# Kernel tuning notes

Measured on AMD Instinct MI355X. Metric: run time of the kernel, lower is better.

The kernel has to match this reference:

```python
import jax, jax.numpy as jnp
import numpy as np

HEAD_DIM = 64
NUM_HEADS = 16
ROPE_BASE = 10000.0


def _rope_cos_sin(seq_len, head_dim, dtype):
    inv_freq = 1.0 / (ROPE_BASE ** (jnp.arange(0, head_dim, 2, dtype=jnp.float32) / head_dim))
    t = jnp.arange(seq_len, dtype=jnp.float32)
    freqs = jnp.outer(t, inv_freq)                      # [S, D/2]
    emb = jnp.concatenate([freqs, freqs], axis=-1)      # [S, D]
    return jnp.cos(emb).astype(dtype), jnp.sin(emb).astype(dtype)


def _rotate_half(x):
    x1, x2 = jnp.split(x, 2, axis=-1)
    return jnp.concatenate([-x2, x1], axis=-1)


def setup_inputs() -> dict:
    key = jax.random.key(0)
    ks = jax.random.split(key, 5)
    B, S, H = 2, 2048, 1024
    x = jax.random.normal(ks[0], (B, S, H), dtype=jnp.float32)
    attention_mask = jnp.ones((B, S), dtype=jnp.float32)
    scale = 0.02
    Wq = jax.random.normal(ks[1], (H, H), dtype=jnp.float32) * scale
    Wk = jax.random.normal(ks[2], (H, H), dtype=jnp.float32) * scale
    Wv = jax.random.normal(ks[3], (H, H), dtype=jnp.float32) * scale
    Wo = jax.random.normal(ks[4], (H, H), dtype=jnp.float32) * scale
    return {"x": x, "attention_mask": attention_mask, "Wq": Wq, "Wk": Wk, "Wv": Wv, "Wo": Wo}


def reference(x, attention_mask, Wq, Wk, Wv, Wo):
    B, S, H = x.shape
    nh, hd = NUM_HEADS, HEAD_DIM
    scale = hd ** -0.5

    # nn.Linear semantics: y = x @ W^T  (W is [out, in])
    q = jnp.einsum('bsh,oh->bso', x, Wq).reshape(B, S, nh, hd).transpose(0, 2, 1, 3)
    k = jnp.einsum('bsh,oh->bso', x, Wk).reshape(B, S, nh, hd).transpose(0, 2, 1, 3)
    v = jnp.einsum('bsh,oh->bso', x, Wv).reshape(B, S, nh, hd).transpose(0, 2, 1, 3)

    cos, sin = _rope_cos_sin(S, hd, x.dtype)            # [S, hd]
    cos = cos[None, None, :, :]
    sin = sin[None, None, :, :]
    q = q * cos + _rotate_half(q) * sin
    k = k * cos + _rotate_half(k) * sin

    attn = jnp.einsum('bhqd,bhkd->bhqk', q, k) * scale  # [B, nh, S, S]
    mask = (1.0 - attention_mask.astype(x.dtype))[:, None, None, :] * jnp.finfo(x.dtype).min
    attn = attn + mask
    attn = jax.nn.softmax(attn, axis=-1)
    out = jnp.einsum('bhqk,bhkd->bhqd', attn, v)        # [B, nh, S, hd]
    out = out.transpose(0, 2, 1, 3).reshape(B, S, nh * hd)
    return jnp.einsum('bso,ho->bsh', out, Wo)
```

## Files before the change

kernel.cpp:

```cpp
#include <hip/hip_runtime.h>
#include <math.h>

#define BB 2
#define SS 2048
#define HH 1024
#define NH 16
#define HD 64
#define MM (BB*SS)

typedef __attribute__((ext_vector_type(8))) _Float16 f16x8;
typedef __attribute__((ext_vector_type(2))) __fp16 hf16x2;
typedef __attribute__((ext_vector_type(4))) float f32x4;

#define QSCALE 0.18033688011112042f

__device__ __forceinline__ unsigned short f2h(float f) {
    union { _Float16 h; unsigned short u; } c;
    c.h = (_Float16)f;
    return c.u;
}

__device__ __forceinline__ unsigned int pkh(float a, float b) {
    union { hf16x2 h; unsigned int u; } c;
    c.h = __builtin_amdgcn_cvt_pkrtz(a, b);
    return c.u;
}

__device__ __forceinline__ void gld16(const void* g, void* s) {
    __builtin_amdgcn_global_load_lds(
        (const __attribute__((address_space(1))) void*)g,
        (__attribute__((address_space(3))) void*)s, 16, 0, 0);
}

__global__ __launch_bounds__(256) void prep(
    const float* __restrict__ x, const float* __restrict__ mask,
    const float* __restrict__ Wq, const float* __restrict__ Wk,
    const float* __restrict__ Wv, const float* __restrict__ Wo,
    unsigned short* __restrict__ xf, unsigned short* __restrict__ wf,
    float* __restrict__ ctab, float* __restrict__ stab, float* __restrict__ mt,
    unsigned int* __restrict__ mflag)
{
    int gtid = blockIdx.x * 256 + threadIdx.x;
    if (gtid < SS * 32) {
        int s = gtid >> 5, i = gtid & 31;
        double invf = pow(10000.0, -(double)i / 32.0);
        double a = (double)s * invf;
        ctab[gtid] = (float)cos(a);
        stab[gtid] = (float)sin(a);
    }
    if (gtid < BB * SS) {
        float mv = mask[gtid];
        mt[gtid] = (1.0f - mv) * (-1.0e38f);
        unsigned long long bal = __ballot(mv == 1.0f);
        if ((threadIdx.x & 63) == 0)
            mflag[gtid >> 6] = (bal == ~0ull) ? 1u : 0u;
    }
    for (int it = gtid; it < 2097152; it += 524288) {
        float4 v; unsigned short* d; size_t off;
        if (it < 1048576) {
            off = (size_t)it * 4;
            v = *(const float4*)(x + off);
            d = xf;
        } else {
            off = (size_t)(it - 1048576) * 4;
            int row = (int)(off >> 10);
            const float* W = row < 1024 ? Wq : row < 2048 ? Wk : row < 3072 ? Wv : Wo;
            v = *(const float4*)(W + (((size_t)(row & 1023)) << 10) + (off & 1023));
            d = wf;
        }
        *(ushort4*)(d + off) = make_ushort4(f2h(v.x), f2h(v.y), f2h(v.z), f2h(v.w));
    }
}

template<int MODE>
__global__ __launch_bounds__(256, 3) void gemm3(
    const unsigned short* __restrict__ Axf,
    const unsigned short* __restrict__ Wf,
    const float* __restrict__ ctab, const float* __restrict__ stab,
    unsigned short* __restrict__ qo, unsigned short* __restrict__ ko,
    unsigned short* __restrict__ vo, float* __restrict__ fout)
{
    __shared__ __align__(16) short lsA[2][128*32];
    __shared__ __align__(16) short lsB[2][128*32];

    const int t = threadIdx.x;
    const int m0 = blockIdx.x * 128;
    const int brow0 = (MODE == 0 ? 0 : 3072) + blockIdx.y * 128;
    const int lane = t & 63, wv = t >> 6;
    const int wm = (wv >> 1) * 64, wn = (wv & 1) * 64;
    const int fr = lane & 15, fg = lane >> 4;

    const int srow = t >> 2, pc = t & 3;
    const int scx = (pc ^ ((srow >> 1) & 3)) * 8;
    const int lo  = srow * 32 + pc * 8;
    const size_t gA0 = (size_t)(m0 + srow) * HH + scx;
    const size_t gA1 = (size_t)(m0 + 64 + srow) * HH + scx;
    const size_t gB0 = (size_t)(brow0 + srow) * HH + scx;
    const size_t gB1 = (size_t)(brow0 + 64 + srow) * HH + scx;

    f32x4 acc[4][4] = {};

#define STAGE(sel, kk) do { \
        gld16(Axf + gA0 + (kk), &lsA[sel][lo]);            \
        gld16(Wf  + gB0 + (kk), &lsB[sel][lo]);            \
        gld16(Axf + gA1 + (kk), &lsA[sel][lo + 64*32]);    \
        gld16(Wf  + gB1 + (kk), &lsB[sel][lo + 64*32]);    \
    } while (0)

    STAGE(0, 0);
    __syncthreads();

    int cur = 0;
    for (int k0 = 0; k0 < HH; k0 += 32) {
        if (k0 + 32 < HH) STAGE(cur ^ 1, k0 + 32);

        f16x8 ah[4], bh[4];
        const int swz = (fg ^ ((fr >> 1) & 3)) * 8;
        #pragma unroll
        for (int mi = 0; mi < 4; ++mi)
            ah[mi] = *(const f16x8*)&lsA[cur][(wm + 16*mi + fr)*32 + swz];
        #pragma unroll
        for (int ni = 0; ni < 4; ++ni)
            bh[ni] = *(const f16x8*)&lsB[cur][(wn + 16*ni + fr)*32 + swz];

        __builtin_amdgcn_s_setprio(1);
        #pragma unroll
        for (int mi = 0; mi < 4; ++mi)
            #pragma unroll
            for (int ni = 0; ni < 4; ++ni)
                acc[mi][ni] = __builtin_amdgcn_mfma_f32_16x16x32_f16(ah[mi], bh[ni], acc[mi][ni], 0, 0, 0);
        __builtin_amdgcn_s_setprio(0);
        __syncthreads();
        cur ^= 1;
    }
#undef STAGE

    if (MODE == 0) {
        const int mat = brow0 >> 10;
        const int obase = (brow0 & 1023) + wn;
        const int h = obase >> 6;
        #pragma unroll
        for (int mi = 0; mi < 4; ++mi)
            #pragma unroll
            for (int rr = 0; rr < 4; ++rr) {
                int m = m0 + wm + 16*mi + 4*fg + rr;
                int b = m >> 11, s = m & (SS - 1);
                float v[4];
                #pragma unroll
                for (int ni = 0; ni < 4; ++ni) v[ni] = acc[mi][ni][rr];
                if (mat < 2) {
                    #pragma unroll
                    for (int ni = 0; ni < 2; ++ni) {
                        int i = 16*ni + fr;
                        float c = ctab[s*32 + i], sn = stab[s*32 + i];
                        float v1 = v[ni], v2 = v[ni + 2];
                        v[ni]     = v1*c - v2*sn;
                        v[ni + 2] = v2*c + v1*sn;
                    }
                }
                if (mat == 0) {
                    #pragma unroll
                    for (int ni = 0; ni < 4; ++ni) v[ni] *= QSCALE;
                }
                size_t base = ((size_t)(b*NH + h) * SS + s) * HD;
                #pragma unroll
                for (int ni = 0; ni < 4; ++ni) {
                    int d = 16*ni + fr;
                    unsigned short hb = f2h(v[ni]);
                    if (mat == 0)      qo[base + d] = hb;
                    else if (mat == 1) ko[base + (d ^ ((s & 7) << 3))] = hb;
                    else {
                        size_t va = ((size_t)(b*NH + h) * HD + d) * SS
                                  + (s & ~63) + ((s & 63) ^ ((d & 7) << 3));
                        vo[va] = hb;
                    }
                }
            }
    } else {
        const int n0 = blockIdx.y * 128 + wn;
        #pragma unroll
        for (int mi = 0; mi < 4; ++mi)
            #pragma unroll
            for (int rr = 0; rr < 4; ++rr) {
                int m = m0 + wm + 16*mi + 4*fg + rr;
                #pragma unroll
                for (int ni = 0; ni < 4; ++ni)
                    fout[(size_t)m * HH + n0 + 16*ni + fr] = acc[mi][ni][rr];
            }
    }
}

__global__ __launch_bounds__(256, 3) void attn(
    const unsigned short* __restrict__ qg, const unsigned short* __restrict__ kg,
    const unsigned short* __restrict__ vtg, const float* __restrict__ mt,
    const unsigned int* __restrict__ mfl, unsigned short* __restrict__ cf)
{
    __shared__ __align__(16) short Ks[2][64*64];
    __shared__ __align__(16) short Vs[2][64*64];
    __shared__ __align__(16) short Ps[128*64];

    const int t = threadIdx.x, lane = t & 63, wv = t >> 6;
    const int fr = lane & 15, fg = lane >> 4, frx = fr & 7;
    const int flat = blockIdx.x;
    const int bh = (flat & 7) + ((flat >> 7) << 3);
    const int q0 = ((flat >> 3) & 15) * 128;
    const int b = bh >> 4, h = bh & 15;

    const unsigned short* kgb = kg  + (size_t)bh*SS*HD;
    const unsigned short* vgb = vtg + (size_t)bh*HD*SS;
    const float* mtb = mt + (size_t)b*SS;
    const unsigned int* mfb = mfl + b*32;

    f16x8 qa[2][2];
    #pragma unroll
    for (int mi = 0; mi < 2; ++mi)
        #pragma unroll
        for (int kc = 0; kc < 2; ++kc)
            qa[mi][kc] = *(const f16x8*)&qg[((size_t)bh*SS + q0 + 32*wv + 16*mi + fr)*HD + kc*32 + fg*8];

    f16x8 onev;
    #pragma unroll
    for (int i = 0; i < 8; ++i) onev[i] = (_Float16)1.0f;

    f32x4 o[2][4] = {};
    f32x4 oS[2] = {};
    int pb[2];
    #pragma unroll
    for (int mi = 0; mi < 2; ++mi) pb[mi] = (32*wv + 16*mi + fr) * 64;
    const int hs = (fr >> 3) * 4;

    const int srow = t >> 3, sg = t & 7;

    gld16(kgb + (size_t)srow*HD + sg*8,      &Ks[0][srow*64 + sg*8]);
    gld16(kgb + (size_t)(32+srow)*HD + sg*8, &Ks[0][(32+srow)*64 + sg*8]);
    gld16(vgb + (size_t)srow*SS + sg*8,      &Vs[0][srow*64 + sg*8]);
    gld16(vgb + (size_t)(32+srow)*SS + sg*8, &Vs[0][(32+srow)*64 + sg*8]);
    __syncthreads();

    int cur = 0;
    for (int kt = 0; kt < SS/64; ++kt) {
        const int k0 = kt * 64;
        if (kt + 1 < SS/64) {
            const int kn = k0 + 64;
            gld16(kgb + (size_t)(kn+srow)*HD + sg*8,      &Ks[cur^1][srow*64 + sg*8]);
            gld16(kgb + (size_t)(kn+32+srow)*HD + sg*8,   &Ks[cur^1][(32+srow)*64 + sg*8]);
            gld16(vgb + (size_t)srow*SS + kn + sg*8,      &Vs[cur^1][srow*64 + sg*8]);
            gld16(vgb + (size_t)(32+srow)*SS + kn + sg*8, &Vs[cur^1][(32+srow)*64 + sg*8]);
        }
        const int fl = __builtin_amdgcn_readfirstlane(mfb[kt]);

        f32x4 sc[2][4] = {};
        __builtin_amdgcn_s_setprio(1);
        #pragma unroll
        for (int kc = 0; kc < 2; ++kc) {
            #pragma unroll
            for (int nf = 0; nf < 4; ++nf) {
                int gr = (4*kc + fg) ^ frx;
                f16x8 kb = *(const f16x8*)&Ks[cur][(16*nf + fr)*64 + gr*8];
                #pragma unroll
                for (int mi = 0; mi < 2; ++mi)
                    sc[mi][nf] = __builtin_amdgcn_mfma_f32_16x16x32_f16(kb, qa[mi][kc], sc[mi][nf], 0, 0, 0);
            }
        }
        __builtin_amdgcn_s_setprio(0);

        if (fl) {
            #pragma unroll
            for (int mi = 0; mi < 2; ++mi)
                #pragma unroll
                for (int nf = 0; nf < 4; ++nf) {
                    float p0 = __builtin_amdgcn_exp2f(sc[mi][nf][0]);
                    float p1 = __builtin_amdgcn_exp2f(sc[mi][nf][1]);
                    float p2 = __builtin_amdgcn_exp2f(sc[mi][nf][2]);
                    float p3 = __builtin_amdgcn_exp2f(sc[mi][nf][3]);
                    uint2 w; w.x = pkh(p0, p1); w.y = pkh(p2, p3);
                    *(uint2*)&Ps[pb[mi] + (((2*nf + (fg >> 1)) ^ frx) * 8) + (4*(fg & 1) ^ hs)] = w;
                }
        } else {
            #pragma unroll
            for (int mi = 0; mi < 2; ++mi)
                #pragma unroll
                for (int nf = 0; nf < 4; ++nf) {
                    float4 m4 = *(const float4*)&mtb[k0 + 16*nf + 4*fg];
                    float p0 = __builtin_amdgcn_exp2f(sc[mi][nf][0] + m4.x);
                    float p1 = __builtin_amdgcn_exp2f(sc[mi][nf][1] + m4.y);
                    float p2 = __builtin_amdgcn_exp2f(sc[mi][nf][2] + m4.z);
                    float p3 = __builtin_amdgcn_exp2f(sc[mi][nf][3] + m4.w);
                    uint2 w; w.x = pkh(p0, p1); w.y = pkh(p2, p3);
                    *(uint2*)&Ps[pb[mi] + (((2*nf + (fg >> 1)) ^ frx) * 8) + (4*(fg & 1) ^ hs)] = w;
                }
        }

        __builtin_amdgcn_s_setprio(1);
        #pragma unroll
        for (int kc = 0; kc < 2; ++kc) {
            const int gr = (4*kc + fg) ^ frx;
            f16x8 pa[2];
            #pragma unroll
            for (int mi = 0; mi < 2; ++mi) {
                int pg = pb[mi] + gr*8;
                union { f16x8 v; uint2 q[2]; } pu;
                pu.q[0] = *(const uint2*)&Ps[pg + hs];
                pu.q[1] = *(const uint2*)&Ps[pg + (hs ^ 4)];
                pa[mi] = pu.v;
            }
            #pragma unroll
            for (int df = 0; df < 4; ++df) {
                f16x8 vb = *(const f16x8*)&Vs[cur][(16*df + fr)*64 + gr*8];
                #pragma unroll
                for (int mi = 0; mi < 2; ++mi)
                    o[mi][df] = __builtin_amdgcn_mfma_f32_16x16x32_f16(vb, pa[mi], o[mi][df], 0, 0, 0);
            }
            #pragma unroll
            for (int mi = 0; mi < 2; ++mi)
                oS[mi] = __builtin_amdgcn_mfma_f32_16x16x32_f16(onev, pa[mi], oS[mi], 0, 0, 0);
        }
        __builtin_amdgcn_s_setprio(0);
        __syncthreads();
        cur ^= 1;
    }

    #pragma unroll
    for (int mi = 0; mi < 2; ++mi) {
        float inv = 1.0f / oS[mi][0];
        size_t base = ((size_t)b*SS + q0 + 32*wv + 16*mi + fr)*HH + h*HD;
        #pragma unroll
        for (int df = 0; df < 4; ++df) {
            uint2 w;
            w.x = pkh(o[mi][df][0]*inv, o[mi][df][1]*inv);
            w.y = pkh(o[mi][df][2]*inv, o[mi][df][3]*inv);
            *(uint2*)&cf[base + 16*df + 4*fg] = w;
        }
    }
}

extern "C" void kernel_launch(void* const* d_in, const int* in_sizes, int n_in,
                              void* d_out, int out_size, void* d_ws, size_t ws_size,
                              hipStream_t stream) {
    const float* x    = (const float*)d_in[0];
    const float* mask = (const float*)d_in[1];
    const float* Wq   = (const float*)d_in[2];
    const float* Wk   = (const float*)d_in[3];
    const float* Wv   = (const float*)d_in[4];
    const float* Wo   = (const float*)d_in[5];
    float* out = (float*)d_out;

    const size_t T = (size_t)MM * HH;
    unsigned short* xf = (unsigned short*)d_ws;
    unsigned short* wf = xf + T;
    unsigned short* qt = wf + T;
    unsigned short* kt = qt + T;
    unsigned short* vt = kt + T;
    float* ctab = (float*)(vt + T);
    float* stab = ctab + SS*32;
    float* mt   = stab + SS*32;
    unsigned int* mfg = (unsigned int*)(mt + BB*SS);
    unsigned short* cf = xf;

    prep<<<2048, 256, 0, stream>>>(x, mask, Wq, Wk, Wv, Wo, xf, wf, ctab, stab, mt, mfg);
    gemm3<0><<<dim3(MM/128, 3*HH/128), 256, 0, stream>>>(xf, wf, ctab, stab,
                                                         qt, kt, vt, nullptr);
    attn<<<512, 256, 0, stream>>>(qt, kt, vt, mt, mfg, cf);
    gemm3<1><<<dim3(MM/128, HH/128), 256, 0, stream>>>(cf, wf, nullptr, nullptr,
                                                       nullptr, nullptr, nullptr, out);
}
```

Before: 113.8 us.

## Split attention waves across key halves with register-reused Q/K/V fragments

Reorganises the attention kernel so each wave owns 64 queries and one half of each 64-key tile, instead of 32 queries over the full tile. K, V and P fragments are loaded once into registers and reused across four query fragments. The row sum is accumulated in scalar registers, replacing the extra ones-vector MFMA. Partial outputs and sums from the two key halves are combined through shared memory at the end. This adds register pressure, so the occupancy hint drops from 3 to 2 blocks per SIMD, and the reduction adds extra syncs.

```diff
diff --git a/kernel.cpp b/kernel.cpp
--- a/kernel.cpp
+++ b/kernel.cpp
@@ -190,7 +190,7 @@
     }
 }
 
-__global__ __launch_bounds__(256, 3) void attn(
+__global__ __launch_bounds__(256, 2) void attn(
     const unsigned short* __restrict__ qg, const unsigned short* __restrict__ kg,
     const unsigned short* __restrict__ vtg, const float* __restrict__ mt,
     const unsigned int* __restrict__ mfl, unsigned short* __restrict__ cf)
@@ -201,6 +201,7 @@
 
     const int t = threadIdx.x, lane = t & 63, wv = t >> 6;
     const int fr = lane & 15, fg = lane >> 4, frx = fr & 7;
+    const int qh = wv & 1, kh = wv >> 1;
     const int flat = blockIdx.x;
     const int bh = (flat & 7) + ((flat >> 7) << 3);
     const int q0 = ((flat >> 3) & 15) * 128;
@@ -211,23 +212,15 @@
     const float* mtb = mt + (size_t)b*SS;
     const unsigned int* mfb = mfl + b*32;
 
-    f16x8 qa[2][2];
+    f16x8 qa[4][2];
     #pragma unroll
-    for (int mi = 0; mi < 2; ++mi)
-        #pragma unroll
-        for (int kc = 0; kc < 2; ++kc)
-            qa[mi][kc] = *(const f16x8*)&qg[((size_t)bh*SS + q0 + 32*wv + 16*mi + fr)*HD + kc*32 + fg*8];
-
-    f16x8 onev;
-    #pragma unroll
-    for (int i = 0; i < 8; ++i) onev[i] = (_Float16)1.0f;
-
-    f32x4 o[2][4] = {};
-    f32x4 oS[2] = {};
-    int pb[2];
-    #pragma unroll
-    for (int mi = 0; mi < 2; ++mi) pb[mi] = (32*wv + 16*mi + fr) * 64;
-    const int hs = (fr >> 3) * 4;
+    for (int qf = 0; qf < 4; ++qf)
+        #pragma unroll
+        for (int dc = 0; dc < 2; ++dc)
+            qa[qf][dc] = *(const f16x8*)&qg[((size_t)bh*SS + q0 + 64*qh + 16*qf + fr)*HD + 32*dc + 8*fg];
+
+    f32x4 o[4][4] = {};
+    float lpart[4] = {0.f, 0.f, 0.f, 0.f};
 
     const int srow = t >> 3, sg = t & 7;
 
@@ -249,88 +242,114 @@
         }
         const int fl = __builtin_amdgcn_readfirstlane(mfb[kt]);
 
+        f16x8 kb[2][2];
+        #pragma unroll
+        for (int nk = 0; nk < 2; ++nk)
+            #pragma unroll
+            for (int dc = 0; dc < 2; ++dc)
+                kb[nk][dc] = *(const f16x8*)&Ks[cur][(32*kh + 16*nk + fr)*64 + (((4*dc + fg) ^ frx) * 8)];
+
         f32x4 sc[2][4] = {};
         __builtin_amdgcn_s_setprio(1);
         #pragma unroll
-        for (int kc = 0; kc < 2; ++kc) {
-            #pragma unroll
-            for (int nf = 0; nf < 4; ++nf) {
-                int gr = (4*kc + fg) ^ frx;
-                f16x8 kb = *(const f16x8*)&Ks[cur][(16*nf + fr)*64 + gr*8];
-                #pragma unroll
-                for (int mi = 0; mi < 2; ++mi)
-                    sc[mi][nf] = __builtin_amdgcn_mfma_f32_16x16x32_f16(kb, qa[mi][kc], sc[mi][nf], 0, 0, 0);
+        for (int dc = 0; dc < 2; ++dc)
+            #pragma unroll
+            for (int nk = 0; nk < 2; ++nk)
+                #pragma unroll
+                for (int qf = 0; qf < 4; ++qf)
+                    sc[nk][qf] = __builtin_amdgcn_mfma_f32_16x16x32_f16(kb[nk][dc], qa[qf][dc], sc[nk][qf], 0, 0, 0);
+        __builtin_amdgcn_s_setprio(0);
+
+        #pragma unroll
+        for (int nk = 0; nk < 2; ++nk) {
+            float4 m4;
+            if (!fl) m4 = *(const float4*)&mtb[k0 + 32*kh + 16*nk + 4*fg];
+            const int pgw = ((4*kh + 2*nk + (fg >> 1)) ^ frx) * 8 + 4*(fg & 1);
+            #pragma unroll
+            for (int qf = 0; qf < 4; ++qf) {
+                float p0, p1, p2, p3;
+                if (fl) {
+                    p0 = __builtin_amdgcn_exp2f(sc[nk][qf][0]);
+                    p1 = __builtin_amdgcn_exp2f(sc[nk][qf][1]);
+                    p2 = __builtin_amdgcn_exp2f(sc[nk][qf][2]);
+                    p3 = __builtin_amdgcn_exp2f(sc[nk][qf][3]);
+                } else {
+                    p0 = __builtin_amdgcn_exp2f(sc[nk][qf][0] + m4.x);
+                    p1 = __builtin_amdgcn_exp2f(sc[nk][qf][1] + m4.y);
+                    p2 = __builtin_amdgcn_exp2f(sc[nk][qf][2] + m4.z);
+                    p3 = __builtin_amdgcn_exp2f(sc[nk][qf][3] + m4.w);
+                }
+                lpart[qf] += (p0 + p1) + (p2 + p3);
+                uint2 w; w.x = pkh(p0, p1); w.y = pkh(p2, p3);
+                *(uint2*)&Ps[(64*qh + 16*qf + fr)*64 + pgw] = w;
             }
         }
-        __builtin_amdgcn_s_setprio(0);
-
-        if (fl) {
-            #pragma unroll
-            for (int mi = 0; mi < 2; ++mi)
-                #pragma unroll
-                for (int nf = 0; nf < 4; ++nf) {
-                    float p0 = __builtin_amdgcn_exp2f(sc[mi][nf][0]);
-                    float p1 = __builtin_amdgcn_exp2f(sc[mi][nf][1]);
-                    float p2 = __builtin_amdgcn_exp2f(sc[mi][nf][2]);
-                    float p3 = __builtin_amdgcn_exp2f(sc[mi][nf][3]);
-                    uint2 w; w.x = pkh(p0, p1); w.y = pkh(p2, p3);
-                    *(uint2*)&Ps[pb[mi] + (((2*nf + (fg >> 1)) ^ frx) * 8) + (4*(fg & 1) ^ hs)] = w;
-                }
-        } else {
-            #pragma unroll
-            for (int mi = 0; mi < 2; ++mi)
-                #pragma unroll
-                for (int nf = 0; nf < 4; ++nf) {
-                    float4 m4 = *(const float4*)&mtb[k0 + 16*nf + 4*fg];
-                    float p0 = __builtin_amdgcn_exp2f(sc[mi][nf][0] + m4.x);
-                    float p1 = __builtin_amdgcn_exp2f(sc[mi][nf][1] + m4.y);
-                    float p2 = __builtin_amdgcn_exp2f(sc[mi][nf][2] + m4.z);
-                    float p3 = __builtin_amdgcn_exp2f(sc[mi][nf][3] + m4.w);
-                    uint2 w; w.x = pkh(p0, p1); w.y = pkh(p2, p3);
-                    *(uint2*)&Ps[pb[mi] + (((2*nf + (fg >> 1)) ^ frx) * 8) + (4*(fg & 1) ^ hs)] = w;
-                }
-        }
-
+
+        const int gr = ((4*kh + fg) ^ frx) * 8;
+        f16x8 vb[4], pa[4];
+        #pragma unroll
+        for (int df = 0; df < 4; ++df)
+            vb[df] = *(const f16x8*)&Vs[cur][(16*df + fr)*64 + gr];
+        #pragma unroll
+        for (int qf = 0; qf < 4; ++qf)
+            pa[qf] = *(const f16x8*)&Ps[(64*qh + 16*qf + fr)*64 + gr];
         __builtin_amdgcn_s_setprio(1);
         #pragma unroll
-        for (int kc = 0; kc < 2; ++kc) {
-            const int gr = (4*kc + fg) ^ frx;
-            f16x8 pa[2];
-            #pragma unroll
-            for (int mi = 0; mi < 2; ++mi) {
-                int pg = pb[mi] + gr*8;
-                union { f16x8 v; uint2 q[2]; } pu;
-                pu.q[0] = *(const uint2*)&Ps[pg + hs];
-                pu.q[1] = *(const uint2*)&Ps[pg + (hs ^ 4)];
-                pa[mi] = pu.v;
-            }
-            #pragma unroll
-            for (int df = 0; df < 4; ++df) {
-                f16x8 vb = *(const f16x8*)&Vs[cur][(16*df + fr)*64 + gr*8];
-                #pragma unroll
-                for (int mi = 0; mi < 2; ++mi)
-                    o[mi][df] = __builtin_amdgcn_mfma_f32_16x16x32_f16(vb, pa[mi], o[mi][df], 0, 0, 0);
-            }
-            #pragma unroll
-            for (int mi = 0; mi < 2; ++mi)
-                oS[mi] = __builtin_amdgcn_mfma_f32_16x16x32_f16(onev, pa[mi], oS[mi], 0, 0, 0);
-        }
+        for (int df = 0; df < 4; ++df)
+            #pragma unroll
+            for (int qf = 0; qf < 4; ++qf)
+                o[df][qf] = __builtin_amdgcn_mfma_f32_16x16x32_f16(vb[df], pa[qf], o[df][qf], 0, 0, 0);
         __builtin_amdgcn_s_setprio(0);
         __syncthreads();
         cur ^= 1;
     }
 
+    float* fx = (float*)Ps;
+    const int xl = qh*64 + lane;
+
+    if (kh) {
+        #pragma unroll
+        for (int qf = 0; qf < 4; ++qf) fx[xl*4 + qf] = lpart[qf];
+    }
+    __syncthreads();
+    float inv[4];
+    if (!kh) {
+        #pragma unroll
+        for (int qf = 0; qf < 4; ++qf) {
+            float l = lpart[qf] + fx[xl*4 + qf];
+            l += __shfl_xor(l, 16);
+            l += __shfl_xor(l, 32);
+            inv[qf] = 1.0f / l;
+        }
+    }
+    __syncthreads();
+
     #pragma unroll
-    for (int mi = 0; mi < 2; ++mi) {
-        float inv = 1.0f / oS[mi][0];
-        size_t base = ((size_t)b*SS + q0 + 32*wv + 16*mi + fr)*HH + h*HD;
-        #pragma unroll
-        for (int df = 0; df < 4; ++df) {
-            uint2 w;
-            w.x = pkh(o[mi][df][0]*inv, o[mi][df][1]*inv);
-            w.y = pkh(o[mi][df][2]*inv, o[mi][df][3]*inv);
-            *(uint2*)&cf[base + 16*df + 4*fg] = w;
-        }
+    for (int half = 0; half < 2; ++half) {
+        if (kh) {
+            #pragma unroll
+            for (int d2 = 0; d2 < 2; ++d2)
+                #pragma unroll
+                for (int qf = 0; qf < 4; ++qf)
+                    *(f32x4*)&fx[(xl*8 + d2*4 + qf)*4] = o[half*2 + d2][qf];
+        }
+        __syncthreads();
+        if (!kh) {
+            #pragma unroll
+            for (int d2 = 0; d2 < 2; ++d2)
+                #pragma unroll
+                for (int qf = 0; qf < 4; ++qf) {
+                    int df = half*2 + d2;
+                    f32x4 r = o[df][qf] + *(const f32x4*)&fx[(xl*8 + d2*4 + qf)*4];
+                    float iv = inv[qf];
+                    uint2 w;
+                    w.x = pkh(r[0]*iv, r[1]*iv);
+                    w.y = pkh(r[2]*iv, r[3]*iv);
+                    size_t base = ((size_t)b*SS + q0 + 64*qh + 16*qf + fr)*HH + h*HD;
+                    *(uint2*)&cf[base + 16*df + 4*fg] = w;
+                }
+        }
+        __syncthreads();
     }
 }
 
```

New measurement: 119.5 us. +5.0%, slower.

## Switch attention to 32x32x16 MFMA with register-resident P via permlane swap

Applied to the files above, without the earlier changes.

Rewrites the attention inner loop to use 32x32x16 MFMA tiles instead of 16x16x32. The probability tile is repacked in registers with v_permlane32_swap rather than round-tripped through LDS, which removes the Ps shared buffer and its stores and loads. The row sum is now accumulated with scalar adds plus one cross-half shuffle, replacing the extra ones-vector MFMA. Larger accumulators raise register pressure, so launch bounds drop from 3 to 2 blocks per SM, which risks lower occupancy.

```diff
diff --git a/kernel.cpp b/kernel.cpp
--- a/kernel.cpp
+++ b/kernel.cpp
@@ -11,6 +11,7 @@
 typedef __attribute__((ext_vector_type(8))) _Float16 f16x8;
 typedef __attribute__((ext_vector_type(2))) __fp16 hf16x2;
 typedef __attribute__((ext_vector_type(4))) float f32x4;
+typedef __attribute__((ext_vector_type(16))) float f32x16;
 
 #define QSCALE 0.18033688011112042f
 
@@ -190,17 +191,18 @@
     }
 }
 
-__global__ __launch_bounds__(256, 3) void attn(
+__global__ __launch_bounds__(256, 2) void attn(
     const unsigned short* __restrict__ qg, const unsigned short* __restrict__ kg,
     const unsigned short* __restrict__ vtg, const float* __restrict__ mt,
     const unsigned int* __restrict__ mfl, unsigned short* __restrict__ cf)
 {
     __shared__ __align__(16) short Ks[2][64*64];
     __shared__ __align__(16) short Vs[2][64*64];
-    __shared__ __align__(16) short Ps[128*64];
 
     const int t = threadIdx.x, lane = t & 63, wv = t >> 6;
-    const int fr = lane & 15, fg = lane >> 4, frx = fr & 7;
+    const int ql = lane & 31;
+    const int u  = lane >> 5;
+    const int qx = ql & 7;
     const int flat = blockIdx.x;
     const int bh = (flat & 7) + ((flat >> 7) << 3);
     const int q0 = ((flat >> 3) & 15) * 128;
@@ -211,23 +213,13 @@
     const float* mtb = mt + (size_t)b*SS;
     const unsigned int* mfb = mfl + b*32;
 
-    f16x8 qa[2][2];
+    f16x8 qa[4];
     #pragma unroll
-    for (int mi = 0; mi < 2; ++mi)
-        #pragma unroll
-        for (int kc = 0; kc < 2; ++kc)
-            qa[mi][kc] = *(const f16x8*)&qg[((size_t)bh*SS + q0 + 32*wv + 16*mi + fr)*HD + kc*32 + fg*8];
-
-    f16x8 onev;
-    #pragma unroll
-    for (int i = 0; i < 8; ++i) onev[i] = (_Float16)1.0f;
-
-    f32x4 o[2][4] = {};
-    f32x4 oS[2] = {};
-    int pb[2];
-    #pragma unroll
-    for (int mi = 0; mi < 2; ++mi) pb[mi] = (32*wv + 16*mi + fr) * 64;
-    const int hs = (fr >> 3) * 4;
+    for (int dc = 0; dc < 4; ++dc)
+        qa[dc] = *(const f16x8*)&qg[((size_t)bh*SS + q0 + 32*wv + ql)*HD + 16*dc + 8*u];
+
+    f32x16 o[2] = {};
+    float lpart = 0.f;
 
     const int srow = t >> 3, sg = t & 7;
 
@@ -249,89 +241,87 @@
         }
         const int fl = __builtin_amdgcn_readfirstlane(mfb[kt]);
 
-        f32x4 sc[2][4] = {};
+        f16x8 kb[2][4];
+        #pragma unroll
+        for (int ktl = 0; ktl < 2; ++ktl)
+            #pragma unroll
+            for (int dc = 0; dc < 4; ++dc)
+                kb[ktl][dc] = *(const f16x8*)&Ks[cur][(32*ktl + ql)*64 + ((2*dc + u) ^ qx)*8];
+
+        f32x16 sc[2] = {};
         __builtin_amdgcn_s_setprio(1);
         #pragma unroll
-        for (int kc = 0; kc < 2; ++kc) {
-            #pragma unroll
-            for (int nf = 0; nf < 4; ++nf) {
-                int gr = (4*kc + fg) ^ frx;
-                f16x8 kb = *(const f16x8*)&Ks[cur][(16*nf + fr)*64 + gr*8];
-                #pragma unroll
-                for (int mi = 0; mi < 2; ++mi)
-                    sc[mi][nf] = __builtin_amdgcn_mfma_f32_16x16x32_f16(kb, qa[mi][kc], sc[mi][nf], 0, 0, 0);
-            }
-        }
+        for (int dc = 0; dc < 4; ++dc)
+            #pragma unroll
+            for (int ktl = 0; ktl < 2; ++ktl)
+                sc[ktl] = __builtin_amdgcn_mfma_f32_32x32x16_f16(kb[ktl][dc], qa[dc], sc[ktl], 0, 0, 0);
         __builtin_amdgcn_s_setprio(0);
 
+        f16x8 vb[2][4];
+        #pragma unroll
+        for (int dt = 0; dt < 2; ++dt)
+            #pragma unroll
+            for (int ki = 0; ki < 4; ++ki)
+                vb[dt][ki] = *(const f16x8*)&Vs[cur][(32*dt + ql)*64 + ((2*ki + u) ^ qx)*8];
+
         if (fl) {
             #pragma unroll
-            for (int mi = 0; mi < 2; ++mi)
-                #pragma unroll
-                for (int nf = 0; nf < 4; ++nf) {
-                    float p0 = __builtin_amdgcn_exp2f(sc[mi][nf][0]);
-                    float p1 = __builtin_amdgcn_exp2f(sc[mi][nf][1]);
-                    float p2 = __builtin_amdgcn_exp2f(sc[mi][nf][2]);
-                    float p3 = __builtin_amdgcn_exp2f(sc[mi][nf][3]);
-                    uint2 w; w.x = pkh(p0, p1); w.y = pkh(p2, p3);
-                    *(uint2*)&Ps[pb[mi] + (((2*nf + (fg >> 1)) ^ frx) * 8) + (4*(fg & 1) ^ hs)] = w;
+            for (int ktl = 0; ktl < 2; ++ktl)
+                #pragma unroll
+                for (int r = 0; r < 16; ++r) {
+                    float p = __builtin_amdgcn_exp2f(sc[ktl][r]);
+                    sc[ktl][r] = p;
+                    lpart += p;
                 }
         } else {
             #pragma unroll
-            for (int mi = 0; mi < 2; ++mi)
-                #pragma unroll
-                for (int nf = 0; nf < 4; ++nf) {
-                    float4 m4 = *(const float4*)&mtb[k0 + 16*nf + 4*fg];
-                    float p0 = __builtin_amdgcn_exp2f(sc[mi][nf][0] + m4.x);
-                    float p1 = __builtin_amdgcn_exp2f(sc[mi][nf][1] + m4.y);
-                    float p2 = __builtin_amdgcn_exp2f(sc[mi][nf][2] + m4.z);
-                    float p3 = __builtin_amdgcn_exp2f(sc[mi][nf][3] + m4.w);
-                    uint2 w; w.x = pkh(p0, p1); w.y = pkh(p2, p3);
-                    *(uint2*)&Ps[pb[mi] + (((2*nf + (fg >> 1)) ^ frx) * 8) + (4*(fg & 1) ^ hs)] = w;
+            for (int ktl = 0; ktl < 2; ++ktl)
+                #pragma unroll
+                for (int g = 0; g < 4; ++g) {
+                    float4 m4 = *(const float4*)&mtb[k0 + 32*ktl + 8*g + 4*u];
+                    #pragma unroll
+                    for (int j = 0; j < 4; ++j) {
+                        float p = __builtin_amdgcn_exp2f(sc[ktl][4*g + j] + (&m4.x)[j]);
+                        sc[ktl][4*g + j] = p;
+                        lpart += p;
+                    }
                 }
         }
 
         __builtin_amdgcn_s_setprio(1);
         #pragma unroll
-        for (int kc = 0; kc < 2; ++kc) {
-            const int gr = (4*kc + fg) ^ frx;
-            f16x8 pa[2];
-            #pragma unroll
-            for (int mi = 0; mi < 2; ++mi) {
-                int pg = pb[mi] + gr*8;
-                union { f16x8 v; uint2 q[2]; } pu;
-                pu.q[0] = *(const uint2*)&Ps[pg + hs];
-                pu.q[1] = *(const uint2*)&Ps[pg + (hs ^ 4)];
-                pa[mi] = pu.v;
-            }
-            #pragma unroll
-            for (int df = 0; df < 4; ++df) {
-                f16x8 vb = *(const f16x8*)&Vs[cur][(16*df + fr)*64 + gr*8];
-                #pragma unroll
-                for (int mi = 0; mi < 2; ++mi)
-                    o[mi][df] = __builtin_amdgcn_mfma_f32_16x16x32_f16(vb, pa[mi], o[mi][df], 0, 0, 0);
-            }
-            #pragma unroll
-            for (int mi = 0; mi < 2; ++mi)
-                oS[mi] = __builtin_amdgcn_mfma_f32_16x16x32_f16(onev, pa[mi], oS[mi], 0, 0, 0);
+        for (int ki = 0; ki < 4; ++ki) {
+            const int ktl = ki >> 1;
+            const int R0 = 8 * (ki & 1);
+            unsigned int A0 = pkh(sc[ktl][R0+0], sc[ktl][R0+1]);
+            unsigned int A1 = pkh(sc[ktl][R0+2], sc[ktl][R0+3]);
+            unsigned int B0 = pkh(sc[ktl][R0+4], sc[ktl][R0+5]);
+            unsigned int B1 = pkh(sc[ktl][R0+6], sc[ktl][R0+7]);
+            asm volatile("v_permlane32_swap_b32 %0, %1" : "+v"(A0), "+v"(B0));
+            asm volatile("v_permlane32_swap_b32 %0, %1" : "+v"(A1), "+v"(B1));
+            union { unsigned int w[4]; f16x8 v; } pf;
+            pf.w[0] = A0; pf.w[1] = A1; pf.w[2] = B0; pf.w[3] = B1;
+            #pragma unroll
+            for (int dt = 0; dt < 2; ++dt)
+                o[dt] = __builtin_amdgcn_mfma_f32_32x32x16_f16(vb[dt][ki], pf.v, o[dt], 0, 0, 0);
         }
         __builtin_amdgcn_s_setprio(0);
         __syncthreads();
         cur ^= 1;
     }
 
+    float l = lpart + __shfl_xor(lpart, 32);
+    float inv = 1.0f / l;
+    size_t base = ((size_t)b*SS + q0 + 32*wv + ql)*HH + h*HD;
     #pragma unroll
-    for (int mi = 0; mi < 2; ++mi) {
-        float inv = 1.0f / oS[mi][0];
-        size_t base = ((size_t)b*SS + q0 + 32*wv + 16*mi + fr)*HH + h*HD;
-        #pragma unroll
-        for (int df = 0; df < 4; ++df) {
+    for (int dt = 0; dt < 2; ++dt)
+        #pragma unroll
+        for (int g = 0; g < 4; ++g) {
             uint2 w;
-            w.x = pkh(o[mi][df][0]*inv, o[mi][df][1]*inv);
-            w.y = pkh(o[mi][df][2]*inv, o[mi][df][3]*inv);
-            *(uint2*)&cf[base + 16*df + 4*fg] = w;
-        }
-    }
+            w.x = pkh(o[dt][4*g+0]*inv, o[dt][4*g+1]*inv);
+            w.y = pkh(o[dt][4*g+2]*inv, o[dt][4*g+3]*inv);
+            *(uint2*)&cf[base + 32*dt + 8*g + 4*u] = w;
+        }
 }
 
 extern "C" void kernel_launch(void* const* d_in, const int* in_sizes, int n_in,
```

Result: no change. 114.5 us (+0.6%).
